# Kernel optimization log

Hardware: AMD Instinct MI355X
Metric: run time of the kernel (lower is better)

The kernel has to match this reference:

```python
import jax, jax.numpy as jnp
import numpy as np

QB = 127.0  # 8-bit activation quant range
EPS = 1e-5


def _bitlinear(x, w, b):
    # BitNet b1.58-style BitLinear.
    # Activation: per-token absmax 8-bit quantization (STE).
    s = QB / jnp.clip(jnp.max(jnp.abs(x), axis=-1, keepdims=True), EPS)
    xq = jnp.clip(jnp.round(x * s), -QB - 1.0, QB) / s
    xq = x + jax.lax.stop_gradient(xq - x)
    # Weight: ternary {-1,0,1} with absmean scaling (STE).
    ws = 1.0 / jnp.clip(jnp.mean(jnp.abs(w)), EPS)
    wq = jnp.clip(jnp.round(w * ws), -1.0, 1.0) / ws
    wq = w + jax.lax.stop_gradient(wq - w)
    return jnp.einsum('bsf,of->bso', xq, wq) + b


def setup_inputs() -> dict:
    key = jax.random.key(0)
    k1, k2, k3, k4, k5, k6 = jax.random.split(key, 6)
    B, S, F = 8, 32768, 128
    evidence = jax.random.normal(k1, (B, S, F), dtype=jnp.float32)
    prior_belief = jax.random.uniform(k2, (B, S, F), dtype=jnp.float32)
    # belief_update params: Linear(2F -> F), Linear(F -> F)
    W1 = jax.random.normal(k3, (F, 2 * F), dtype=jnp.float32) * (1.0 / np.sqrt(2 * F))
    b1 = jax.random.normal(k4, (F,), dtype=jnp.float32) * 0.01
    W2 = jax.random.normal(k5, (F, F), dtype=jnp.float32) * (1.0 / np.sqrt(F))
    b2 = jax.random.normal(k6, (F,), dtype=jnp.float32) * 0.01
    return {"evidence": evidence, "prior_belief": prior_belief,
            "W1": W1, "b1": b1, "W2": W2, "b2": b2}


def reference(evidence, prior_belief, W1, b1, W2, b2):
    # update network: BitLinear -> ReLU -> BitLinear -> Sigmoid
    upd_in = jnp.concatenate([prior_belief, evidence], axis=-1)  # [B,S,2F]
    h = jax.nn.relu(_bitlinear(upd_in, W1, b1))                  # [B,S,F]
    likelihood = jax.nn.sigmoid(_bitlinear(h, W2, b2))           # [B,S,F]
    posterior_unnorm = prior_belief * likelihood
    normalizer = jnp.clip(posterior_unnorm.sum(axis=1, keepdims=True), 1e-10)
    return posterior_unnorm / normalizer
```

## Files before the change

kernel.cpp:

```cpp
#include <hip/hip_runtime.h>
#include <hip/hip_bf16.h>
#include <math.h>

typedef int   i32x4 __attribute__((ext_vector_type(4)));
typedef unsigned int u32;

#define QBF 127.0f
#define EPSF 1e-5f
#define FF 128
#define NROWS (8 * 32768)
#define NBLK 512
#define TPB 8

#define W1_OFF    0
#define W2_OFF    32768
#define WBUF_OFF  49152
#define CS_OFF    66560
#define LDS_TOTAL 68608

#define LGKM0() asm volatile("s_waitcnt lgkmcnt(0)" ::: "memory")
#define SB()    __builtin_amdgcn_sched_barrier(0)

static __device__ __forceinline__ float bcast_lane(float v, int lane) {
    return __builtin_bit_cast(float, __builtin_amdgcn_readlane(__builtin_bit_cast(int, v), lane));
}
static __device__ __forceinline__ u32 packi8(float a, float b, float c, float d, float s) {
    int i0 = (int)rintf(a * s), i1 = (int)rintf(b * s);
    int i2 = (int)rintf(c * s), i3 = (int)rintf(d * s);
    return (u32)(i0 & 0xFF) | ((u32)(i1 & 0xFF) << 8) |
           ((u32)(i2 & 0xFF) << 16) | ((u32)i3 << 24);
}

__global__ void pstats_kernel(const float* __restrict__ W1,
                              const float* __restrict__ W2,
                              double* __restrict__ psum) {
    __shared__ double red[256];
    int b = blockIdx.x, t = threadIdx.x;
    const float4* src = (b < 32) ? (const float4*)(W1 + b * 1024)
                                 : (const float4*)(W2 + (b - 32) * 1024);
    float4 v = src[t];
    red[t] = (double)fabsf(v.x) + (double)fabsf(v.y)
           + (double)fabsf(v.z) + (double)fabsf(v.w);
    __syncthreads();
    for (int o = 128; o > 0; o >>= 1) { if (t < o) red[t] += red[t + o]; __syncthreads(); }
    if (t == 0) psum[b] = red[0];
}

__global__ void sfinal_kernel(const double* __restrict__ psum, float* __restrict__ hdr) {
    __shared__ double red[64];
    int t = threadIdx.x;
    red[t] = (t < 32) ? psum[t] : 0.0;
    __syncthreads();
    for (int o = 16; o > 0; o >>= 1) { if (t < o) red[t] += red[t + o]; __syncthreads(); }
    double s1 = red[0];
    __syncthreads();
    red[t] = (t < 16) ? psum[32 + t] : 0.0;
    __syncthreads();
    for (int o = 8; o > 0; o >>= 1) { if (t < o) red[t] += red[t + o]; __syncthreads(); }
    if (t == 0) {
        hdr[0] = 1.0f / fmaxf((float)(s1 * (1.0 / 32768.0)), EPSF);
        hdr[1] = 1.0f / fmaxf((float)(red[0] * (1.0 / 16384.0)), EPSF);
    }
}

__global__ void wquant_kernel(const float* __restrict__ W1,
                              const float* __restrict__ W2,
                              const float* __restrict__ hdr,
                              char* __restrict__ wq) {
    int g = blockIdx.x * 256 + threadIdx.x;
    float ws1 = hdr[0], ws2 = hdr[1];
    const float* src; float wsx; char* dst;
    if (g < 2048) {
        int gi = g >> 6, l = g & 63;
        int ct = gi >> 2, kb = gi & 3;
        src = W1 + (ct * 16 + (l & 15)) * 256 + kb * 64 + (l >> 4) * 16;
        wsx = ws1;
        dst = wq + gi * 1024 + l * 16;
    } else {
        int g2 = g - 2048;
        int gi = g2 >> 6, l = g2 & 63;
        int ct = gi >> 1, kb = gi & 1;
        src = W2 + (ct * 16 + (l & 15)) * 128 + kb * 64 + (l >> 4) * 16;
        wsx = ws2;
        dst = wq + 32768 + gi * 1024 + l * 16;
    }
    u32 o[4];
    #pragma unroll
    for (int q = 0; q < 4; ++q) {
        float4 v = *(const float4*)(src + q * 4);
        float q0 = fminf(fmaxf(rintf(v.x * wsx), -1.f), 1.f);
        float q1 = fminf(fmaxf(rintf(v.y * wsx), -1.f), 1.f);
        float q2 = fminf(fmaxf(rintf(v.z * wsx), -1.f), 1.f);
        float q3 = fminf(fmaxf(rintf(v.w * wsx), -1.f), 1.f);
        o[q] = packi8(q0, q1, q2, q3, 1.0f);
    }
    *(uint4*)dst = make_uint4(o[0], o[1], o[2], o[3]);
}

__global__ __launch_bounds__(256, 2) void fused_kernel(
    const float* __restrict__ evid, const float* __restrict__ prior,
    const float* __restrict__ bias1, const float* __restrict__ bias2,
    const char* __restrict__ wq, const float* __restrict__ hdr,
    float* __restrict__ out, float* __restrict__ partials)
{
    __shared__ __align__(16) char smem[LDS_TOTAL];
    const int tid = threadIdx.x;
    const int w = tid >> 6, l = tid & 63;
    const int lr = l & 15, lg = l >> 4;
    const int lc = l & 31, half = l >> 5;
    char* wbuf = smem + WBUF_OFF + w * 4352;
    float* colsum = (float*)(smem + CS_OFF);
    const float ws1 = hdr[0], ws2 = hdr[1];

    {
        const uint4* g = (const uint4*)wq;
        #pragma unroll
        for (int i = 0; i < 12; ++i) {
            uint4 v = g[i * 256 + tid];
            *(uint4*)(smem + (size_t)(i * 256 + tid) * 16) = v;
        }
    }
    float4 xr[16];
    {
        const float* srcp = half ? evid : prior;
        int R0 = blockIdx.x * 512 + w * 16;
        #pragma unroll
        for (int r = 0; r < 16; ++r)
            xr[r] = *(const float4*)(srcp + (size_t)(R0 + r) * FF + lc * 4);
    }
    __syncthreads();

    float csum[8][4];
    #pragma unroll
    for (int ct = 0; ct < 8; ++ct)
        #pragma unroll
        for (int j = 0; j < 4; ++j) csum[ct][j] = 0.f;

    for (int t = 0; t < TPB; ++t) {
        const int R0c = blockIdx.x * 512 + t * 64 + w * 16;

        #pragma unroll
        for (int r = 0; r < 16; ++r) {
            float4 v = xr[r];
            float m = fmaxf(fmaxf(fabsf(v.x), fabsf(v.y)),
                            fmaxf(fabsf(v.z), fabsf(v.w)));
            *(float*)(wbuf + r * 272 + l * 4) = m;
        }
        LGKM0(); SB();
        float mm;
        {
            const char* p = wbuf + lr * 272 + lg * 64;
            float4 a = *(const float4*)(p);
            float4 b = *(const float4*)(p + 16);
            float4 c = *(const float4*)(p + 32);
            float4 d = *(const float4*)(p + 48);
            float m0 = fmaxf(fmaxf(a.x, a.y), fmaxf(a.z, a.w));
            float m1 = fmaxf(fmaxf(b.x, b.y), fmaxf(b.z, b.w));
            float m2 = fmaxf(fmaxf(c.x, c.y), fmaxf(c.z, c.w));
            float m3 = fmaxf(fmaxf(d.x, d.y), fmaxf(d.z, d.w));
            mm = fmaxf(fmaxf(m0, m1), fmaxf(m2, m3));
        }
        mm = fmaxf(mm, __shfl_xor(mm, 16, 64));
        mm = fmaxf(mm, __shfl_xor(mm, 32, 64));
        const float sA = QBF / fmaxf(mm, EPSF);
        const float rinv1 = 1.0f / (sA * ws1);

        #pragma unroll
        for (int r = 0; r < 16; ++r) {
            float s_r = bcast_lane(sA, r);
            float4 v = xr[r];
            *(u32*)(wbuf + r * 272 + l * 4) = packi8(v.x, v.y, v.z, v.w, s_r);
        }

        if (t + 1 < TPB) {
            const float* srcp = half ? evid : prior;
            int R0n = R0c + 64;
            #pragma unroll
            for (int r = 0; r < 16; ++r)
                xr[r] = *(const float4*)(srcp + (size_t)(R0n + r) * FF + lc * 4);
        }
        LGKM0(); SB();

        i32x4 acc1[8] = {};
        #pragma unroll
        for (int kb = 0; kb < 4; ++kb) {
            i32x4 xb = *(const i32x4*)(wbuf + lr * 272 + kb * 64 + lg * 16);
            #pragma unroll
            for (int ct = 0; ct < 8; ++ct) {
                i32x4 wa = *(const i32x4*)(smem + (ct * 4 + kb) * 1024 + l * 16);
                acc1[ct] = __builtin_amdgcn_mfma_i32_16x16x64_i8(wa, xb, acc1[ct], 0, 0, 0);
            }
        }

        float h[8][4];
        float hmax = 0.f;
        #pragma unroll
        for (int ct = 0; ct < 8; ++ct) {
            float4 b4 = *(const float4*)(bias1 + ct * 16 + lg * 4);
            h[ct][0] = fmaxf((float)acc1[ct][0] * rinv1 + b4.x, 0.f);
            h[ct][1] = fmaxf((float)acc1[ct][1] * rinv1 + b4.y, 0.f);
            h[ct][2] = fmaxf((float)acc1[ct][2] * rinv1 + b4.z, 0.f);
            h[ct][3] = fmaxf((float)acc1[ct][3] * rinv1 + b4.w, 0.f);
            hmax = fmaxf(hmax, fmaxf(fmaxf(h[ct][0], h[ct][1]),
                                     fmaxf(h[ct][2], h[ct][3])));
        }
        hmax = fmaxf(hmax, __shfl_xor(hmax, 16, 64));
        hmax = fmaxf(hmax, __shfl_xor(hmax, 32, 64));
        const float s2 = QBF / fmaxf(hmax, EPSF);
        const float rinv2 = 1.0f / (s2 * ws2);

        #pragma unroll
        for (int ct = 0; ct < 8; ++ct)
            *(u32*)(wbuf + lr * 272 + ct * 16 + lg * 4) =
                packi8(h[ct][0], h[ct][1], h[ct][2], h[ct][3], s2);
        LGKM0(); SB();

        i32x4 acc2[8] = {};
        #pragma unroll
        for (int kb = 0; kb < 2; ++kb) {
            i32x4 hb = *(const i32x4*)(wbuf + lr * 272 + kb * 64 + lg * 16);
            #pragma unroll
            for (int ct = 0; ct < 8; ++ct) {
                i32x4 wa = *(const i32x4*)(smem + W2_OFF + (ct * 2 + kb) * 1024 + l * 16);
                acc2[ct] = __builtin_amdgcn_mfma_i32_16x16x64_i8(wa, hb, acc2[ct], 0, 0, 0);
            }
        }

        const size_t rowoff = (size_t)(R0c + lr) * FF;
        #pragma unroll
        for (int ct = 0; ct < 8; ++ct) {
            float4 b4 = *(const float4*)(bias2 + ct * 16 + lg * 4);
            float4 pv = *(const float4*)(prior + rowoff + ct * 16 + lg * 4);
            float4 un;
            float y0 = (float)acc2[ct][0] * rinv2 + b4.x;
            float y1 = (float)acc2[ct][1] * rinv2 + b4.y;
            float y2 = (float)acc2[ct][2] * rinv2 + b4.z;
            float y3 = (float)acc2[ct][3] * rinv2 + b4.w;
            un.x = pv.x / (1.0f + __expf(-y0));
            un.y = pv.y / (1.0f + __expf(-y1));
            un.z = pv.z / (1.0f + __expf(-y2));
            un.w = pv.w / (1.0f + __expf(-y3));
            *(float4*)(out + rowoff + ct * 16 + lg * 4) = un;
            csum[ct][0] += un.x; csum[ct][1] += un.y;
            csum[ct][2] += un.z; csum[ct][3] += un.w;
        }
    }

    #pragma unroll
    for (int msk = 1; msk < 16; msk <<= 1) {
        #pragma unroll
        for (int ct = 0; ct < 8; ++ct) {
            #pragma unroll
            for (int j = 0; j < 4; ++j)
                csum[ct][j] += __shfl_xor(csum[ct][j], msk, 64);
        }
    }
    if (lr == 0) {
        #pragma unroll
        for (int ct = 0; ct < 8; ++ct) {
            float4 cv;
            cv.x = csum[ct][0]; cv.y = csum[ct][1];
            cv.z = csum[ct][2]; cv.w = csum[ct][3];
            *(float4*)(colsum + w * 128 + ct * 16 + lg * 4) = cv;
        }
    }
    __syncthreads();
    if (tid < FF)
        partials[(size_t)blockIdx.x * FF + tid] =
            colsum[tid] + colsum[128 + tid] + colsum[256 + tid] + colsum[384 + tid];
}

__global__ void norm_kernel(const float* __restrict__ partials, float* __restrict__ norm) {
    __shared__ float red[2][128];
    int b = blockIdx.x;
    int f = threadIdx.x & 127, tg = threadIdx.x >> 7;
    float s = 0.f;
    for (int t = tg * 32; t < tg * 32 + 32; ++t)
        s += partials[((size_t)b * 64 + t) * FF + f];
    red[tg][f] = s; __syncthreads();
    if (tg == 0)
        norm[b * FF + f] = fmaxf(red[0][f] + red[1][f], 1e-10f);
}

__global__ void div_kernel(float* __restrict__ out, const float* __restrict__ norm) {
    size_t i4 = (size_t)blockIdx.x * blockDim.x + threadIdx.x;
    const size_t total4 = (size_t)NROWS * FF / 4;
    for (; i4 < total4; i4 += (size_t)gridDim.x * blockDim.x) {
        size_t i = i4 * 4;
        float4 v = *(float4*)(out + i);
        int b = (int)(i >> 22);
        int f = (int)(i & 127);
        float4 nv = *(const float4*)(norm + b * FF + f);
        v.x /= nv.x; v.y /= nv.y; v.z /= nv.z; v.w /= nv.w;
        *(float4*)(out + i) = v;
    }
}

extern "C" void kernel_launch(void* const* d_in, const int* in_sizes, int n_in,
                              void* d_out, int out_size, void* d_ws, size_t ws_size,
                              hipStream_t stream) {
    const float* evid  = (const float*)d_in[0];
    const float* prior = (const float*)d_in[1];
    const float* W1    = (const float*)d_in[2];
    const float* b1    = (const float*)d_in[3];
    const float* W2    = (const float*)d_in[4];
    const float* b2    = (const float*)d_in[5];
    float* out = (float*)d_out;

    char* ws = (char*)d_ws;
    float*  hdr      = (float*)ws;
    double* psum     = (double*)(ws + 256);
    char*   wq       = ws + 1024;
    float*  partials = (float*)(ws + 65536);
    float*  norm     = (float*)(ws + 65536 + 262144);

    pstats_kernel<<<48, 256, 0, stream>>>(W1, W2, psum);
    sfinal_kernel<<<1, 64, 0, stream>>>(psum, hdr);
    wquant_kernel<<<12, 256, 0, stream>>>(W1, W2, hdr, wq);
    fused_kernel<<<NBLK, 256, 0, stream>>>(evid, prior, b1, b2, wq, hdr, out, partials);
    norm_kernel<<<8, 256, 0, stream>>>(partials, norm);
    div_kernel<<<2048, 256, 0, stream>>>(out, norm);
}
```

Before: 169.1 us.

## Split next-tile prefetch across GEMMs and coalesce output stores via LDS staging

The prefetch of the next tile's 16 input rows is split in two: half is issued before GEMM1 and half after the layer-2 quantized activations are written, which lowers how many prefetch registers are live at the same time. Output stores are staged through the per-wave LDS buffer in two 64-column halves so that each global write covers contiguous 256-byte row segments instead of scattered 16-byte pieces. The sigmoid division is replaced with a hardware reciprocal multiply, which is slightly less precise. The staging adds LDS round trips and extra waits.

```diff
diff --git a/kernel.cpp b/kernel.cpp
--- a/kernel.cpp
+++ b/kernel.cpp
@@ -12,7 +12,6 @@
 #define NBLK 512
 #define TPB 8
 
-#define W1_OFF    0
 #define W2_OFF    32768
 #define WBUF_OFF  49152
 #define CS_OFF    66560
@@ -174,9 +173,9 @@
 
         if (t + 1 < TPB) {
             const float* srcp = half ? evid : prior;
-            int R0n = R0c + 64;
-            #pragma unroll
-            for (int r = 0; r < 16; ++r)
+            int R0n = blockIdx.x * 512 + (t + 1) * 64 + w * 16;
+            #pragma unroll
+            for (int r = 0; r < 8; ++r)
                 xr[r] = *(const float4*)(srcp + (size_t)(R0n + r) * FF + lc * 4);
         }
         LGKM0(); SB();
@@ -213,6 +212,14 @@
         for (int ct = 0; ct < 8; ++ct)
             *(u32*)(wbuf + lr * 272 + ct * 16 + lg * 4) =
                 packi8(h[ct][0], h[ct][1], h[ct][2], h[ct][3], s2);
+
+        if (t + 1 < TPB) {
+            const float* srcp = half ? evid : prior;
+            int R0n = blockIdx.x * 512 + (t + 1) * 64 + w * 16;
+            #pragma unroll
+            for (int r = 8; r < 16; ++r)
+                xr[r] = *(const float4*)(srcp + (size_t)(R0n + r) * FF + lc * 4);
+        }
         LGKM0(); SB();
 
         i32x4 acc2[8] = {};
@@ -228,21 +235,33 @@
 
         const size_t rowoff = (size_t)(R0c + lr) * FF;
         #pragma unroll
-        for (int ct = 0; ct < 8; ++ct) {
-            float4 b4 = *(const float4*)(bias2 + ct * 16 + lg * 4);
-            float4 pv = *(const float4*)(prior + rowoff + ct * 16 + lg * 4);
-            float4 un;
-            float y0 = (float)acc2[ct][0] * rinv2 + b4.x;
-            float y1 = (float)acc2[ct][1] * rinv2 + b4.y;
-            float y2 = (float)acc2[ct][2] * rinv2 + b4.z;
-            float y3 = (float)acc2[ct][3] * rinv2 + b4.w;
-            un.x = pv.x / (1.0f + __expf(-y0));
-            un.y = pv.y / (1.0f + __expf(-y1));
-            un.z = pv.z / (1.0f + __expf(-y2));
-            un.w = pv.w / (1.0f + __expf(-y3));
-            *(float4*)(out + rowoff + ct * 16 + lg * 4) = un;
-            csum[ct][0] += un.x; csum[ct][1] += un.y;
-            csum[ct][2] += un.z; csum[ct][3] += un.w;
+        for (int p = 0; p < 2; ++p) {
+            #pragma unroll
+            for (int c = 0; c < 4; ++c) {
+                const int ct = 4 * p + c;
+                float4 b4 = *(const float4*)(bias2 + ct * 16 + lg * 4);
+                float4 pv = *(const float4*)(prior + rowoff + ct * 16 + lg * 4);
+                float4 un;
+                float y0 = (float)acc2[ct][0] * rinv2 + b4.x;
+                float y1 = (float)acc2[ct][1] * rinv2 + b4.y;
+                float y2 = (float)acc2[ct][2] * rinv2 + b4.z;
+                float y3 = (float)acc2[ct][3] * rinv2 + b4.w;
+                un.x = pv.x * __builtin_amdgcn_rcpf(1.0f + __expf(-y0));
+                un.y = pv.y * __builtin_amdgcn_rcpf(1.0f + __expf(-y1));
+                un.z = pv.z * __builtin_amdgcn_rcpf(1.0f + __expf(-y2));
+                un.w = pv.w * __builtin_amdgcn_rcpf(1.0f + __expf(-y3));
+                csum[ct][0] += un.x; csum[ct][1] += un.y;
+                csum[ct][2] += un.z; csum[ct][3] += un.w;
+                *(float4*)(wbuf + lr * 272 + c * 64 + lg * 16) = un;
+            }
+            LGKM0(); SB();
+            #pragma unroll
+            for (int i = 0; i < 4; ++i) {
+                int rloc = 4 * i + (l >> 4);
+                float4 v = *(const float4*)(wbuf + rloc * 272 + (l & 15) * 16);
+                *(float4*)(out + (size_t)(R0c + rloc) * FF + p * 64 + (l & 15) * 4) = v;
+            }
+            LGKM0(); SB();
         }
     }
 
@@ -265,9 +284,11 @@
         }
     }
     __syncthreads();
-    if (tid < FF)
-        partials[(size_t)blockIdx.x * FF + tid] =
-            colsum[tid] + colsum[128 + tid] + colsum[256 + tid] + colsum[384 + tid];
+    if (tid < FF) {
+        float p = colsum[tid] + colsum[128 + tid]
+                + colsum[256 + tid] + colsum[384 + tid];
+        partials[(size_t)blockIdx.x * FF + tid] = p;
+    }
 }
 
 __global__ void norm_kernel(const float* __restrict__ partials, float* __restrict__ norm) {
```

Result: faster. 159.3 us (-5.8%).
